# Optimization experiments

Hardware: AMD Instinct MI355X
Metric: run time of the kernel (lower is better)

## Reference

```python
import jax, jax.numpy as jnp
import numpy as np

N_AGENTS = 5
RNN = 128
ATT = 64
N_ACT = 10
IN_DIM = 256
SIZE = 65535  # multiple of N_AGENTS -> padding branch never taken
TAU = 0.01


def _gru_cell(x, h, w_ih, w_hh, b_ih, b_hh):
    # PyTorch GRUCell math
    gi = x @ w_ih.T + b_ih
    gh = h @ w_hh.T + b_hh
    i_r, i_z, i_n = jnp.split(gi, 3, axis=-1)
    h_r, h_z, h_n = jnp.split(gh, 3, axis=-1)
    r = jax.nn.sigmoid(i_r + h_r)
    z = jax.nn.sigmoid(i_z + h_z)
    n = jnp.tanh(i_n + r * h_n)
    return (1.0 - z) * n + z * h


def _gru_seq(xs, w_ih, w_hh, b_ih, b_hh):
    # xs: [T, B, D]; zero initial hidden, returns all step outputs [T, B, RNN]
    h0 = jnp.zeros((xs.shape[1], RNN), xs.dtype)
    def step(h, x):
        h2 = _gru_cell(x, h, w_ih, w_hh, b_ih, b_hh)
        return h2, h2
    _, ys = jax.lax.scan(step, h0, xs)
    return ys


def setup_inputs():
    key = jax.random.key(0)
    ks = jax.random.split(key, 26)
    def u(k, shape, fan):
        return jax.random.uniform(k, shape, jnp.float32, -1.0, 1.0) / np.sqrt(fan)
    return {
        'obs': jax.random.normal(ks[0], (SIZE, IN_DIM), jnp.float32),
        'hidden_state': jax.random.normal(ks[1], (SIZE, RNN), jnp.float32),
        'enc_w': u(ks[2], (RNN, IN_DIM), IN_DIM), 'enc_b': u(ks[3], (RNN,), IN_DIM),
        'gru_w_ih': u(ks[4], (3 * RNN, RNN), RNN), 'gru_w_hh': u(ks[5], (3 * RNN, RNN), RNN),
        'gru_b_ih': u(ks[6], (3 * RNN,), RNN), 'gru_b_hh': u(ks[7], (3 * RNN,), RNN),
        'bi_w_ih_f': u(ks[8], (3 * RNN, 2 * RNN), RNN), 'bi_w_hh_f': u(ks[9], (3 * RNN, RNN), RNN),
        'bi_b_ih_f': u(ks[10], (3 * RNN,), RNN), 'bi_b_hh_f': u(ks[11], (3 * RNN,), RNN),
        'bi_w_ih_r': u(ks[12], (3 * RNN, 2 * RNN), RNN), 'bi_w_hh_r': u(ks[13], (3 * RNN, RNN), RNN),
        'bi_b_ih_r': u(ks[14], (3 * RNN,), RNN), 'bi_b_hh_r': u(ks[15], (3 * RNN,), RNN),
        'hard_w': u(ks[16], (2, 2 * RNN), 2 * RNN), 'hard_b': u(ks[17], (2,), 2 * RNN),
        'q_w': u(ks[18], (ATT, RNN), RNN),
        'k_w': u(ks[19], (ATT, RNN), RNN),
        'v_w': u(ks[20], (ATT, RNN), RNN), 'v_b': u(ks[21], (ATT,), RNN),
        'dec_w': u(ks[22], (N_ACT, RNN + ATT), RNN + ATT), 'dec_b': u(ks[23], (N_ACT,), RNN + ATT),
    }


def reference(obs, hidden_state, enc_w, enc_b, gru_w_ih, gru_w_hh, gru_b_ih, gru_b_hh,
              bi_w_ih_f, bi_w_hh_f, bi_b_ih_f, bi_b_hh_f,
              bi_w_ih_r, bi_w_hh_r, bi_b_ih_r, bi_b_hh_r,
              hard_w, hard_b, q_w, k_w, v_w, v_b, dec_w, dec_b):
    size = obs.shape[0]
    bpa = size // N_AGENTS  # batch per agent; SIZE is a multiple of N_AGENTS

    x = jax.nn.relu(obs @ enc_w.T + enc_b)
    h_out = _gru_cell(x, hidden_state, gru_w_ih, gru_w_hh, gru_b_ih, gru_b_hh)

    # --- hard attention: pairwise agent features -> bi-GRU -> gumbel-softmax gate ---
    # (computed exactly as in the original; note the original soft_attention
    #  ignores hard_weights, so this does not influence the returned output)
    h = h_out.reshape(bpa, N_AGENTS, RNN)
    nbr = np.array([[j for j in range(N_AGENTS) if j != i] for i in range(N_AGENTS)])  # [n, n-1]
    h_i = jnp.broadcast_to(h[:, :, None, :], (bpa, N_AGENTS, N_AGENTS - 1, RNN))
    h_j = h[:, nbr, :]                              # [bpa, n, n-1, RNN]
    pair = jnp.concatenate([h_i, h_j], axis=-1)     # [bpa, n, n-1, 2*RNN]
    seq = pair.transpose(2, 0, 1, 3).reshape(N_AGENTS - 1, bpa * N_AGENTS, 2 * RNN)
    fwd = _gru_seq(seq, bi_w_ih_f, bi_w_hh_f, bi_b_ih_f, bi_b_hh_f)
    bwd = _gru_seq(seq[::-1], bi_w_ih_r, bi_w_hh_r, bi_b_ih_r, bi_b_hh_r)[::-1]
    h_hard = jnp.concatenate([fwd, bwd], axis=-1)   # [n-1, B, 2*RNN]
    h_hard = h_hard.transpose(1, 0, 2).reshape(-1, 2 * RNN)
    logits = h_hard @ hard_w.T + hard_b             # [B*(n-1), 2]
    u01 = jax.random.uniform(jax.random.key(42), logits.shape, jnp.float32, 1e-10, 1.0)
    gumbel = -jnp.log(-jnp.log(u01))
    gs = jax.nn.softmax((logits + gumbel) / TAU, axis=-1)
    hard_weights = gs[:, 1].reshape(bpa, N_AGENTS, 1, N_AGENTS - 1).transpose(1, 0, 2, 3)
    _ = hard_weights  # unused downstream, matching the original module

    # --- soft attention: original loops per sample doing a 1x1 matmul+softmax;
    #     vectorized here. softmax over a single element is identically 1. ---
    q = h_out @ q_w.T
    k = h_out @ k_w.T
    v = jax.nn.relu(h_out @ v_w.T + v_b)
    score = jnp.sum(q * k, axis=-1, keepdims=True) / np.sqrt(ATT)  # [B,1]
    soft_w = jax.nn.softmax(score, axis=-1)                         # all ones
    x_att = v * soft_w

    final_input = jnp.concatenate([h_out, x_att], axis=-1)
    output = final_input @ dec_w.T + dec_b
    return output, h_out
```

## Files before the change

### kernel.cpp

```cpp
#include <hip/hip_runtime.h>
#include <stdint.h>

#define SIZE 65535

typedef __bf16 bf16x8 __attribute__((ext_vector_type(8)));
typedef float floatx4 __attribute__((ext_vector_type(4)));

#define WS_ENCW 0
#define WS_WIH  32768
#define WS_WHH  81920
#define WS_VW   131072
#define WS_DECW 139264
#define WS_TOTC 17792

__device__ __forceinline__ unsigned short f2bf(float f) {
    union { float f; unsigned int u; } v; v.f = f;
    unsigned int u = v.u;
    return (unsigned short)((u + 0x7fffu + ((u >> 16) & 1u)) >> 16);
}
__device__ __forceinline__ float bf2f(unsigned short b) {
    union { unsigned int u; float f; } v; v.u = ((unsigned int)b) << 16;
    return v.f;
}
__device__ __forceinline__ float sigmf(float x) {
    x = fminf(fmaxf(x, -30.f), 30.f);
    return 1.f / (1.f + __expf(-x));
}
__device__ __forceinline__ float tanhfast(float x) {
    x = fminf(fmaxf(x, -15.f), 15.f);
    float e = __expf(2.f * x);
    return (e - 1.f) / (e + 1.f);
}

union BF8 { bf16x8 v; unsigned short s[8]; };

__device__ __forceinline__ bf16x8 cvt8g(const float* p) {
    float4 a = *reinterpret_cast<const float4*>(p);
    float4 b = *reinterpret_cast<const float4*>(p + 4);
    BF8 r;
    r.s[0] = f2bf(a.x); r.s[1] = f2bf(a.y); r.s[2] = f2bf(a.z); r.s[3] = f2bf(a.w);
    r.s[4] = f2bf(b.x); r.s[5] = f2bf(b.y); r.s[6] = f2bf(b.z); r.s[7] = f2bf(b.w);
    return r.v;
}
__device__ __forceinline__ bf16x8 ld8(const unsigned short* p) {
    return *reinterpret_cast<const bf16x8*>(p);
}

__global__ __launch_bounds__(256) void cvt_weights(
    const float* __restrict__ enc_w, const float* __restrict__ w_ih,
    const float* __restrict__ w_hh, const float* __restrict__ v_w,
    const float* __restrict__ dec_w, unsigned short* __restrict__ ws) {
    int c = blockIdx.x * 256 + threadIdx.x;
    if (c >= WS_TOTC) return;
    const int lane = c & 63;
    const int l = lane & 15;
    const int q = lane >> 4;
    const float* src; int row, col, stride; bool zero = false;
    if (c < 4096) {
        int lt = c >> 6; int nt = lt >> 3, kt = lt & 7;
        row = nt * 16 + l; col = kt * 32 + q * 8; src = enc_w; stride = 256;
    } else if (c < 10240) {
        int lt = (c - 4096) >> 6; int nt = lt / 12; int r2 = lt % 12;
        int g = r2 >> 2, kt = r2 & 3;
        row = g * 128 + nt * 16 + l; col = kt * 32 + q * 8; src = w_ih; stride = 128;
    } else if (c < 16384) {
        int lt = (c - 10240) >> 6; int nt = lt / 12; int r2 = lt % 12;
        int g = r2 >> 2, kt = r2 & 3;
        row = g * 128 + nt * 16 + l; col = kt * 32 + q * 8; src = w_hh; stride = 128;
    } else if (c < 17408) {
        int lt = (c - 16384) >> 6; int nt = lt >> 2, kt = lt & 3;
        row = nt * 16 + l; col = kt * 32 + q * 8; src = v_w; stride = 128;
    } else {
        int kt = (c - 17408) >> 6;
        row = l; col = kt * 32 + q * 8; src = dec_w; stride = 192;
        zero = (l >= 10);
    }
    float4 a, b;
    if (zero) { a = make_float4(0.f,0.f,0.f,0.f); b = a; }
    else {
        const float* p = src + (size_t)row * stride + col;
        a = *reinterpret_cast<const float4*>(p);
        b = *reinterpret_cast<const float4*>(p + 4);
    }
    unsigned short* d = ws + (size_t)c * 8;
    d[0]=f2bf(a.x); d[1]=f2bf(a.y); d[2]=f2bf(a.z); d[3]=f2bf(a.w);
    d[4]=f2bf(b.x); d[5]=f2bf(b.y); d[6]=f2bf(b.z); d[7]=f2bf(b.w);
}

__global__ __launch_bounds__(256, 2) void attn_critic_kernel(
    const float* __restrict__ obs,
    const float* __restrict__ hid,
    const float* __restrict__ enc_b,
    const float* __restrict__ b_ih,
    const float* __restrict__ b_hh,
    const float* __restrict__ v_b,
    const float* __restrict__ dec_b,
    const unsigned short* __restrict__ wsw,
    float* __restrict__ out)
{
    __shared__ __align__(16) unsigned short sA[4][32][136];
    __shared__ __align__(16) unsigned short sV[4][32][72];
    __shared__ __align__(16) float sO[4][32][10];

    const int tid  = threadIdx.x;
    const int wave = tid >> 6;
    const int lane = tid & 63;
    const int l15  = lane & 15;
    const int quad = lane >> 4;
    const int wrow0 = (blockIdx.x * 4 + wave) * 32;

    int rA0 = wrow0 + l15;      rA0 = (rA0 < SIZE) ? rA0 : (SIZE - 1);
    int rA1 = wrow0 + 16 + l15; rA1 = (rA1 < SIZE) ? rA1 : (SIZE - 1);

    bf16x8 aob[2][8], hf[2][4];
    {
        const float* o0 = obs + (size_t)rA0 * 256;
        const float* o1 = obs + (size_t)rA1 * 256;
#pragma unroll
        for (int kt = 0; kt < 8; ++kt) {
            aob[0][kt] = cvt8g(o0 + kt * 32 + quad * 8);
            aob[1][kt] = cvt8g(o1 + kt * 32 + quad * 8);
        }
        const float* h0 = hid + (size_t)rA0 * 128;
        const float* h1 = hid + (size_t)rA1 * 128;
#pragma unroll
        for (int kt = 0; kt < 4; ++kt) {
            hf[0][kt] = cvt8g(h0 + kt * 32 + quad * 8);
            hf[1][kt] = cvt8g(h1 + kt * 32 + quad * 8);
        }
    }
    __builtin_amdgcn_sched_barrier(0);

    {
        const unsigned short* encf = wsw + WS_ENCW + lane * 8;
#pragma unroll 2
        for (int nt = 0; nt < 8; ++nt) {
            floatx4 a0 = floatx4{0.f,0.f,0.f,0.f}, a1 = a0;
#pragma unroll
            for (int kt = 0; kt < 8; ++kt) {
                bf16x8 b = ld8(encf + (size_t)(nt * 8 + kt) * 512);
                a0 = __builtin_amdgcn_mfma_f32_16x16x32_bf16(aob[0][kt], b, a0, 0, 0, 0);
                a1 = __builtin_amdgcn_mfma_f32_16x16x32_bf16(aob[1][kt], b, a1, 0, 0, 0);
            }
            float bias = enc_b[nt * 16 + l15];
#pragma unroll
            for (int r = 0; r < 4; ++r) {
                sA[wave][quad * 4 + r][nt * 16 + l15]      = f2bf(fmaxf(a0[r] + bias, 0.f));
                sA[wave][16 + quad * 4 + r][nt * 16 + l15] = f2bf(fmaxf(a1[r] + bias, 0.f));
            }
        }
    }
    bf16x8 xf[2][4];
#pragma unroll
    for (int kt = 0; kt < 4; ++kt) {
        xf[0][kt] = ld8(&sA[wave][l15][kt * 32 + quad * 8]);
        xf[1][kt] = ld8(&sA[wave][16 + l15][kt * 32 + quad * 8]);
    }

    {
        const unsigned short* wihf = wsw + WS_WIH + lane * 8;
        const unsigned short* whhf = wsw + WS_WHH + lane * 8;
#pragma unroll 1
        for (int nt = 0; nt < 8; ++nt) {
            const int nr = nt * 16 + l15;
            floatx4 gi[3][2], gh[3][2];
#pragma unroll
            for (int g = 0; g < 3; ++g) {
                gi[g][0] = floatx4{0.f,0.f,0.f,0.f}; gi[g][1] = gi[g][0];
                gh[g][0] = gi[g][0]; gh[g][1] = gi[g][0];
            }
#pragma unroll
            for (int g = 0; g < 3; ++g)
#pragma unroll
                for (int kt = 0; kt < 4; ++kt) {
                    bf16x8 bi = ld8(wihf + (size_t)((nt * 3 + g) * 4 + kt) * 512);
                    bf16x8 bh = ld8(whhf + (size_t)((nt * 3 + g) * 4 + kt) * 512);
                    gi[g][0] = __builtin_amdgcn_mfma_f32_16x16x32_bf16(xf[0][kt], bi, gi[g][0], 0, 0, 0);
                    gi[g][1] = __builtin_amdgcn_mfma_f32_16x16x32_bf16(xf[1][kt], bi, gi[g][1], 0, 0, 0);
                    gh[g][0] = __builtin_amdgcn_mfma_f32_16x16x32_bf16(hf[0][kt], bh, gh[g][0], 0, 0, 0);
                    gh[g][1] = __builtin_amdgcn_mfma_f32_16x16x32_bf16(hf[1][kt], bh, gh[g][1], 0, 0, 0);
                }
            const float bir_ = b_ih[nr], biz_ = b_ih[nr + 128], bin_ = b_ih[nr + 256];
            const float bhr_ = b_hh[nr], bhz_ = b_hh[nr + 128], bhn_ = b_hh[nr + 256];
#pragma unroll
            for (int m = 0; m < 2; ++m)
#pragma unroll
                for (int r = 0; r < 4; ++r) {
                    const int grow = wrow0 + m * 16 + quad * 4 + r;
                    const int rowc = (grow < SIZE) ? grow : (SIZE - 1);
                    float hprev = hid[(size_t)rowc * 128 + nr];
                    float rg = sigmf(gi[0][m][r] + bir_ + gh[0][m][r] + bhr_);
                    float zg = sigmf(gi[1][m][r] + biz_ + gh[1][m][r] + bhz_);
                    float ng = tanhfast(gi[2][m][r] + bin_ + rg * (gh[2][m][r] + bhn_));
                    float ho = (1.f - zg) * ng + zg * hprev;
                    sA[wave][m * 16 + quad * 4 + r][nr] = f2bf(ho);
                }
        }
    }

    {
        float* out_h = out + (size_t)SIZE * 10;
#pragma unroll 1
        for (int it = 0; it < 16; ++it) {
            int idx = it * 256 + lane * 4;
            int rr = idx >> 7, cc = idx & 127;
            int grow = wrow0 + rr;
            if (grow < SIZE) {
                float2 p0 = make_float2(bf2f(sA[wave][rr][cc]),     bf2f(sA[wave][rr][cc + 1]));
                float2 p1 = make_float2(bf2f(sA[wave][rr][cc + 2]), bf2f(sA[wave][rr][cc + 3]));
                float* dst = out_h + (size_t)grow * 128 + cc;
                *reinterpret_cast<float2*>(dst)     = p0;
                *reinterpret_cast<float2*>(dst + 2) = p1;
            }
        }
    }

    bf16x8 af[2][4];
#pragma unroll
    for (int kt = 0; kt < 4; ++kt) {
        af[0][kt] = ld8(&sA[wave][l15][kt * 32 + quad * 8]);
        af[1][kt] = ld8(&sA[wave][16 + l15][kt * 32 + quad * 8]);
    }
    {
        const unsigned short* vwf = wsw + WS_VW + lane * 8;
#pragma unroll 1
        for (int nt = 0; nt < 4; ++nt) {
            floatx4 a0 = floatx4{0.f,0.f,0.f,0.f}, a1 = a0;
#pragma unroll
            for (int kt = 0; kt < 4; ++kt) {
                bf16x8 b = ld8(vwf + (size_t)(nt * 4 + kt) * 512);
                a0 = __builtin_amdgcn_mfma_f32_16x16x32_bf16(af[0][kt], b, a0, 0, 0, 0);
                a1 = __builtin_amdgcn_mfma_f32_16x16x32_bf16(af[1][kt], b, a1, 0, 0, 0);
            }
            float bias = v_b[nt * 16 + l15];
#pragma unroll
            for (int r = 0; r < 4; ++r) {
                sV[wave][quad * 4 + r][nt * 16 + l15]      = f2bf(fmaxf(a0[r] + bias, 0.f));
                sV[wave][16 + quad * 4 + r][nt * 16 + l15] = f2bf(fmaxf(a1[r] + bias, 0.f));
            }
        }
    }

    {
        const unsigned short* decf = wsw + WS_DECW + lane * 8;
        floatx4 d0 = floatx4{0.f,0.f,0.f,0.f}, d1 = d0;
#pragma unroll
        for (int kt = 0; kt < 6; ++kt) {
            bf16x8 b = ld8(decf + (size_t)kt * 512);
            bf16x8 a0 = (kt < 4) ? af[0][kt] : ld8(&sV[wave][l15][(kt - 4) * 32 + quad * 8]);
            bf16x8 a1 = (kt < 4) ? af[1][kt] : ld8(&sV[wave][16 + l15][(kt - 4) * 32 + quad * 8]);
            d0 = __builtin_amdgcn_mfma_f32_16x16x32_bf16(a0, b, d0, 0, 0, 0);
            d1 = __builtin_amdgcn_mfma_f32_16x16x32_bf16(a1, b, d1, 0, 0, 0);
        }
        if (l15 < 10) {
            float bias = dec_b[l15];
#pragma unroll
            for (int r = 0; r < 4; ++r) {
                sO[wave][quad * 4 + r][l15]      = d0[r] + bias;
                sO[wave][16 + quad * 4 + r][l15] = d1[r] + bias;
            }
        }
#pragma unroll
        for (int j = 0; j < 5; ++j) {
            int idx = j * 64 + lane;
            int row = idx / 10, col = idx % 10;
            int grow = wrow0 + row;
            if (grow < SIZE)
                out[(size_t)grow * 10 + col] = sO[wave][row][col];
        }
    }
}

extern "C" void kernel_launch(void* const* d_in, const int* in_sizes, int n_in,
                              void* d_out, int out_size, void* d_ws, size_t ws_size,
                              hipStream_t stream) {
    const float* obs   = (const float*)d_in[0];
    const float* hid   = (const float*)d_in[1];
    const float* enc_w = (const float*)d_in[2];
    const float* enc_b = (const float*)d_in[3];
    const float* w_ih  = (const float*)d_in[4];
    const float* w_hh  = (const float*)d_in[5];
    const float* b_ih  = (const float*)d_in[6];
    const float* b_hh  = (const float*)d_in[7];
    const float* v_w   = (const float*)d_in[20];
    const float* v_b   = (const float*)d_in[21];
    const float* dec_w = (const float*)d_in[22];
    const float* dec_b = (const float*)d_in[23];
    unsigned short* wsw = (unsigned short*)d_ws;
    float* out = (float*)d_out;

    hipLaunchKernelGGL(cvt_weights, dim3((WS_TOTC + 255) / 256), dim3(256), 0, stream,
                       enc_w, w_ih, w_hh, v_w, dec_w, wsw);
    hipLaunchKernelGGL(attn_critic_kernel, dim3(512), dim3(256), 0, stream,
                       obs, hid, enc_b, b_ih, b_hh, v_b, dec_b, wsw, out);
}
```

Baseline: 224.1 us.

## Split fused critic kernel into three passes with LDS-staged weights

Replaces the single fused kernel with three kernels: an encoder pass that writes bf16 activations to workspace, a GRU pass that splits output columns across four blocks per row tile, and a value/decoder pass that reads back the fp32 hidden output. Each pass stages its weights into LDS via global_load_lds instead of streaming them from global/L2 per wave, and the GRU pass swaps operand order so the output layout allows vectorized float4 stores. This removes the repeated per-wave global weight reads and the serialized long-lived register footprint, at the cost of extra global round trips for the intermediate x and h_out, re-reading hid four times, and added launch overhead.

New measurement: 234.4 us. +4.6%, slower.

```diff
diff --git a/kernel.cpp b/kernel.cpp
--- a/kernel.cpp
+++ b/kernel.cpp
@@ -11,16 +11,13 @@
 #define WS_WHH  81920
 #define WS_VW   131072
 #define WS_DECW 139264
-#define WS_TOTC 17792
+#define WS_TOTC 17920
+#define X_WS    143360
 
 __device__ __forceinline__ unsigned short f2bf(float f) {
     union { float f; unsigned int u; } v; v.f = f;
     unsigned int u = v.u;
     return (unsigned short)((u + 0x7fffu + ((u >> 16) & 1u)) >> 16);
-}
-__device__ __forceinline__ float bf2f(unsigned short b) {
-    union { unsigned int u; float f; } v; v.u = ((unsigned int)b) << 16;
-    return v.f;
 }
 __device__ __forceinline__ float sigmf(float x) {
     x = fminf(fmaxf(x, -30.f), 30.f);
@@ -44,6 +41,11 @@
 }
 __device__ __forceinline__ bf16x8 ld8(const unsigned short* p) {
     return *reinterpret_cast<const bf16x8*>(p);
+}
+__device__ __forceinline__ void glds16(const unsigned short* g, unsigned short* l) {
+    __builtin_amdgcn_global_load_lds(
+        (const __attribute__((address_space(1))) unsigned int*)g,
+        (__attribute__((address_space(3))) unsigned int*)l, 16, 0, 0);
 }
 
 __global__ __launch_bounds__(256) void cvt_weights(
@@ -73,7 +75,7 @@
     } else {
         int kt = (c - 17408) >> 6;
         row = l; col = kt * 32 + q * 8; src = dec_w; stride = 192;
-        zero = (l >= 10);
+        zero = (l >= 10) || (kt >= 6);
     }
     float4 a, b;
     if (zero) { a = make_float4(0.f,0.f,0.f,0.f); b = a; }
@@ -87,18 +89,176 @@
     d[4]=f2bf(b.x); d[5]=f2bf(b.y); d[6]=f2bf(b.z); d[7]=f2bf(b.w);
 }
 
-__global__ __launch_bounds__(256, 2) void attn_critic_kernel(
+__global__ __launch_bounds__(256, 2) void pass1_enc(
     const float* __restrict__ obs,
+    const float* __restrict__ enc_b,
+    const unsigned short* __restrict__ wsw,
+    unsigned short* __restrict__ xws)
+{
+    __shared__ __align__(16) unsigned short wenc[32768];
+
+    const int tid  = threadIdx.x;
+    const int wave = tid >> 6;
+    const int lane = tid & 63;
+    const int l15  = lane & 15;
+    const int quad = lane >> 4;
+    const int wrow0 = blockIdx.x * 128 + wave * 32;
+
+#pragma unroll
+    for (int s = 0; s < 16; ++s) {
+        const int c = s * 256 + tid;
+        glds16(wsw + WS_ENCW + (size_t)c * 8, wenc + (size_t)c * 8);
+    }
+
+    int rA0 = wrow0 + l15;      rA0 = (rA0 < SIZE) ? rA0 : (SIZE - 1);
+    int rA1 = wrow0 + 16 + l15; rA1 = (rA1 < SIZE) ? rA1 : (SIZE - 1);
+
+    bf16x8 bo[2][8];
+    {
+        const float* o0 = obs + (size_t)rA0 * 256;
+        const float* o1 = obs + (size_t)rA1 * 256;
+#pragma unroll
+        for (int kt = 0; kt < 8; ++kt) {
+            bo[0][kt] = cvt8g(o0 + kt * 32 + quad * 8);
+            bo[1][kt] = cvt8g(o1 + kt * 32 + quad * 8);
+        }
+    }
+    __syncthreads();
+
+#pragma unroll 1
+    for (int nt = 0; nt < 8; ++nt) {
+        floatx4 d0 = floatx4{0.f,0.f,0.f,0.f}, d1 = d0;
+#pragma unroll
+        for (int kt = 0; kt < 8; ++kt) {
+            bf16x8 a = ld8(&wenc[(nt * 8 + kt) * 512 + lane * 8]);
+            d0 = __builtin_amdgcn_mfma_f32_16x16x32_bf16(a, bo[0][kt], d0, 0, 0, 0);
+            d1 = __builtin_amdgcn_mfma_f32_16x16x32_bf16(a, bo[1][kt], d1, 0, 0, 0);
+        }
+        const float4 ebv = *reinterpret_cast<const float4*>(enc_b + nt * 16 + quad * 4);
+        const float eb[4] = {ebv.x, ebv.y, ebv.z, ebv.w};
+#pragma unroll
+        for (int m = 0; m < 2; ++m) {
+            const int grow = wrow0 + m * 16 + l15;
+            if (grow < SIZE) {
+                const floatx4& d = m ? d1 : d0;
+                ushort4 pk;
+                pk.x = f2bf(fmaxf(d[0] + eb[0], 0.f));
+                pk.y = f2bf(fmaxf(d[1] + eb[1], 0.f));
+                pk.z = f2bf(fmaxf(d[2] + eb[2], 0.f));
+                pk.w = f2bf(fmaxf(d[3] + eb[3], 0.f));
+                *reinterpret_cast<ushort4*>(xws + (size_t)grow * 128 + nt * 16 + quad * 4) = pk;
+            }
+        }
+    }
+}
+
+__global__ __launch_bounds__(256, 3) void pass2_gru(
     const float* __restrict__ hid,
-    const float* __restrict__ enc_b,
     const float* __restrict__ b_ih,
     const float* __restrict__ b_hh,
+    const unsigned short* __restrict__ wsw,
+    const unsigned short* __restrict__ xws,
+    float* __restrict__ out_h)
+{
+    __shared__ __align__(16) unsigned short wq[24576];
+
+    const int tid  = threadIdx.x;
+    const int wave = tid >> 6;
+    const int lane = tid & 63;
+    const int l15  = lane & 15;
+    const int quad = lane >> 4;
+    const int q    = blockIdx.x & 3;
+    const int tile = blockIdx.x >> 2;
+    const int wrow0 = tile * 128 + wave * 32;
+
+#pragma unroll
+    for (int s = 0; s < 12; ++s) {
+        const int c = s * 256 + tid;
+        const int f = c >> 6, li = c & 63;
+        int ff = (f < 24) ? f : f - 24;
+        const int ntL = ff / 12, rm = ff % 12;
+        const int g = rm >> 2, kt = rm & 3;
+        const int gidx = (((q * 2 + ntL) * 3 + g) * 4 + kt);
+        const unsigned short* src = wsw + ((f < 24) ? WS_WIH : WS_WHH)
+                                        + (size_t)gidx * 512 + li * 8;
+        glds16(src, wq + (size_t)c * 8);
+    }
+
+    int rA0 = wrow0 + l15;      rA0 = (rA0 < SIZE) ? rA0 : (SIZE - 1);
+    int rA1 = wrow0 + 16 + l15; rA1 = (rA1 < SIZE) ? rA1 : (SIZE - 1);
+
+    bf16x8 xb[2][4], hb[2][4];
+#pragma unroll
+    for (int kt = 0; kt < 4; ++kt) {
+        xb[0][kt] = ld8(xws + (size_t)rA0 * 128 + kt * 32 + quad * 8);
+        xb[1][kt] = ld8(xws + (size_t)rA1 * 128 + kt * 32 + quad * 8);
+        hb[0][kt] = cvt8g(hid + (size_t)rA0 * 128 + kt * 32 + quad * 8);
+        hb[1][kt] = cvt8g(hid + (size_t)rA1 * 128 + kt * 32 + quad * 8);
+    }
+    __syncthreads();
+
+#pragma unroll 1
+    for (int ntL = 0; ntL < 2; ++ntL) {
+        const int oc0 = q * 32 + ntL * 16;
+        floatx4 gi[3][2], gh[3][2];
+#pragma unroll
+        for (int g = 0; g < 3; ++g) {
+            gi[g][0] = floatx4{0.f,0.f,0.f,0.f}; gi[g][1] = gi[g][0];
+            gh[g][0] = gi[g][0]; gh[g][1] = gi[g][0];
+        }
+#pragma unroll
+        for (int g = 0; g < 3; ++g)
+#pragma unroll
+            for (int kt = 0; kt < 4; ++kt) {
+                bf16x8 ai = ld8(&wq[((ntL * 3 + g) * 4 + kt) * 512 + lane * 8]);
+                bf16x8 ah = ld8(&wq[12288 + ((ntL * 3 + g) * 4 + kt) * 512 + lane * 8]);
+                gi[g][0] = __builtin_amdgcn_mfma_f32_16x16x32_bf16(ai, xb[0][kt], gi[g][0], 0, 0, 0);
+                gi[g][1] = __builtin_amdgcn_mfma_f32_16x16x32_bf16(ai, xb[1][kt], gi[g][1], 0, 0, 0);
+                gh[g][0] = __builtin_amdgcn_mfma_f32_16x16x32_bf16(ah, hb[0][kt], gh[g][0], 0, 0, 0);
+                gh[g][1] = __builtin_amdgcn_mfma_f32_16x16x32_bf16(ah, hb[1][kt], gh[g][1], 0, 0, 0);
+            }
+        const float4 birv = *reinterpret_cast<const float4*>(b_ih + oc0 + quad * 4);
+        const float4 bizv = *reinterpret_cast<const float4*>(b_ih + 128 + oc0 + quad * 4);
+        const float4 binv = *reinterpret_cast<const float4*>(b_ih + 256 + oc0 + quad * 4);
+        const float4 bhrv = *reinterpret_cast<const float4*>(b_hh + oc0 + quad * 4);
+        const float4 bhzv = *reinterpret_cast<const float4*>(b_hh + 128 + oc0 + quad * 4);
+        const float4 bhnv = *reinterpret_cast<const float4*>(b_hh + 256 + oc0 + quad * 4);
+        const float bir[4] = {birv.x, birv.y, birv.z, birv.w};
+        const float biz[4] = {bizv.x, bizv.y, bizv.z, bizv.w};
+        const float bin[4] = {binv.x, binv.y, binv.z, binv.w};
+        const float bhr[4] = {bhrv.x, bhrv.y, bhrv.z, bhrv.w};
+        const float bhz[4] = {bhzv.x, bhzv.y, bhzv.z, bhzv.w};
+        const float bhn[4] = {bhnv.x, bhnv.y, bhnv.z, bhnv.w};
+#pragma unroll
+        for (int m = 0; m < 2; ++m) {
+            const int grow = wrow0 + m * 16 + l15;
+            const int rowc = (grow < SIZE) ? grow : (SIZE - 1);
+            const float4 hpv = *reinterpret_cast<const float4*>(hid + (size_t)rowc * 128 + oc0 + quad * 4);
+            const float hp[4] = {hpv.x, hpv.y, hpv.z, hpv.w};
+            float ho[4];
+#pragma unroll
+            for (int r = 0; r < 4; ++r) {
+                float rg = sigmf(gi[0][m][r] + bir[r] + gh[0][m][r] + bhr[r]);
+                float zg = sigmf(gi[1][m][r] + biz[r] + gh[1][m][r] + bhz[r]);
+                float ng = tanhfast(gi[2][m][r] + bin[r] + rg * (gh[2][m][r] + bhn[r]));
+                ho[r] = (1.f - zg) * ng + zg * hp[r];
+            }
+            if (grow < SIZE)
+                *reinterpret_cast<float4*>(out_h + (size_t)grow * 128 + oc0 + quad * 4) =
+                    make_float4(ho[0], ho[1], ho[2], ho[3]);
+        }
+    }
+}
+
+__global__ __launch_bounds__(256, 3) void pass3_vdec(
+    const float* __restrict__ hsrc,
     const float* __restrict__ v_b,
     const float* __restrict__ dec_b,
     const unsigned short* __restrict__ wsw,
     float* __restrict__ out)
 {
-    __shared__ __align__(16) unsigned short sA[4][32][136];
+    __shared__ __align__(16) unsigned short wv[8192];
+    __shared__ __align__(16) unsigned short wdec[4096];
     __shared__ __align__(16) unsigned short sV[4][32][72];
     __shared__ __align__(16) float sO[4][32][10];
 
@@ -107,153 +267,59 @@
     const int lane = tid & 63;
     const int l15  = lane & 15;
     const int quad = lane >> 4;
-    const int wrow0 = (blockIdx.x * 4 + wave) * 32;
+    const int wrow0 = blockIdx.x * 128 + wave * 32;
+
+#pragma unroll
+    for (int s = 0; s < 4; ++s) {
+        const int c = s * 256 + tid;
+        glds16(wsw + WS_VW + (size_t)c * 8, wv + (size_t)c * 8);
+    }
+#pragma unroll
+    for (int s = 0; s < 2; ++s) {
+        const int c = s * 256 + tid;
+        glds16(wsw + WS_DECW + (size_t)c * 8, wdec + (size_t)c * 8);
+    }
 
     int rA0 = wrow0 + l15;      rA0 = (rA0 < SIZE) ? rA0 : (SIZE - 1);
     int rA1 = wrow0 + 16 + l15; rA1 = (rA1 < SIZE) ? rA1 : (SIZE - 1);
 
-    bf16x8 aob[2][8], hf[2][4];
+    bf16x8 ha[2][4];
+#pragma unroll
+    for (int kt = 0; kt < 4; ++kt) {
+        ha[0][kt] = cvt8g(hsrc + (size_t)rA0 * 128 + kt * 32 + quad * 8);
+        ha[1][kt] = cvt8g(hsrc + (size_t)rA1 * 128 + kt * 32 + quad * 8);
+    }
+    __syncthreads();
+
+#pragma unroll 1
+    for (int nt = 0; nt < 4; ++nt) {
+        floatx4 a0 = floatx4{0.f,0.f,0.f,0.f}, a1 = a0;
+#pragma unroll
+        for (int kt = 0; kt < 4; ++kt) {
+            bf16x8 b = ld8(&wv[(nt * 4 + kt) * 512 + lane * 8]);
+            a0 = __builtin_amdgcn_mfma_f32_16x16x32_bf16(ha[0][kt], b, a0, 0, 0, 0);
+            a1 = __builtin_amdgcn_mfma_f32_16x16x32_bf16(ha[1][kt], b, a1, 0, 0, 0);
+        }
+        const float bias = v_b[nt * 16 + l15];
+#pragma unroll
+        for (int r = 0; r < 4; ++r) {
+            sV[wave][quad * 4 + r][nt * 16 + l15]      = f2bf(fmaxf(a0[r] + bias, 0.f));
+            sV[wave][16 + quad * 4 + r][nt * 16 + l15] = f2bf(fmaxf(a1[r] + bias, 0.f));
+        }
+    }
+
     {
-        const float* o0 = obs + (size_t)rA0 * 256;
-        const float* o1 = obs + (size_t)rA1 * 256;
-#pragma unroll
-        for (int kt = 0; kt < 8; ++kt) {
-            aob[0][kt] = cvt8g(o0 + kt * 32 + quad * 8);
-            aob[1][kt] = cvt8g(o1 + kt * 32 + quad * 8);
-        }
-        const float* h0 = hid + (size_t)rA0 * 128;
-        const float* h1 = hid + (size_t)rA1 * 128;
-#pragma unroll
-        for (int kt = 0; kt < 4; ++kt) {
-            hf[0][kt] = cvt8g(h0 + kt * 32 + quad * 8);
-            hf[1][kt] = cvt8g(h1 + kt * 32 + quad * 8);
-        }
-    }
-    __builtin_amdgcn_sched_barrier(0);
-
-    {
-        const unsigned short* encf = wsw + WS_ENCW + lane * 8;
-#pragma unroll 2
-        for (int nt = 0; nt < 8; ++nt) {
-            floatx4 a0 = floatx4{0.f,0.f,0.f,0.f}, a1 = a0;
-#pragma unroll
-            for (int kt = 0; kt < 8; ++kt) {
-                bf16x8 b = ld8(encf + (size_t)(nt * 8 + kt) * 512);
-                a0 = __builtin_amdgcn_mfma_f32_16x16x32_bf16(aob[0][kt], b, a0, 0, 0, 0);
-                a1 = __builtin_amdgcn_mfma_f32_16x16x32_bf16(aob[1][kt], b, a1, 0, 0, 0);
-            }
-            float bias = enc_b[nt * 16 + l15];
-#pragma unroll
-            for (int r = 0; r < 4; ++r) {
-                sA[wave][quad * 4 + r][nt * 16 + l15]      = f2bf(fmaxf(a0[r] + bias, 0.f));
-                sA[wave][16 + quad * 4 + r][nt * 16 + l15] = f2bf(fmaxf(a1[r] + bias, 0.f));
-            }
-        }
-    }
-    bf16x8 xf[2][4];
-#pragma unroll
-    for (int kt = 0; kt < 4; ++kt) {
-        xf[0][kt] = ld8(&sA[wave][l15][kt * 32 + quad * 8]);
-        xf[1][kt] = ld8(&sA[wave][16 + l15][kt * 32 + quad * 8]);
-    }
-
-    {
-        const unsigned short* wihf = wsw + WS_WIH + lane * 8;
-        const unsigned short* whhf = wsw + WS_WHH + lane * 8;
-#pragma unroll 1
-        for (int nt = 0; nt < 8; ++nt) {
-            const int nr = nt * 16 + l15;
-            floatx4 gi[3][2], gh[3][2];
-#pragma unroll
-            for (int g = 0; g < 3; ++g) {
-                gi[g][0] = floatx4{0.f,0.f,0.f,0.f}; gi[g][1] = gi[g][0];
-                gh[g][0] = gi[g][0]; gh[g][1] = gi[g][0];
-            }
-#pragma unroll
-            for (int g = 0; g < 3; ++g)
-#pragma unroll
-                for (int kt = 0; kt < 4; ++kt) {
-                    bf16x8 bi = ld8(wihf + (size_t)((nt * 3 + g) * 4 + kt) * 512);
-                    bf16x8 bh = ld8(whhf + (size_t)((nt * 3 + g) * 4 + kt) * 512);
-                    gi[g][0] = __builtin_amdgcn_mfma_f32_16x16x32_bf16(xf[0][kt], bi, gi[g][0], 0, 0, 0);
-                    gi[g][1] = __builtin_amdgcn_mfma_f32_16x16x32_bf16(xf[1][kt], bi, gi[g][1], 0, 0, 0);
-                    gh[g][0] = __builtin_amdgcn_mfma_f32_16x16x32_bf16(hf[0][kt], bh, gh[g][0], 0, 0, 0);
-                    gh[g][1] = __builtin_amdgcn_mfma_f32_16x16x32_bf16(hf[1][kt], bh, gh[g][1], 0, 0, 0);
-                }
-            const float bir_ = b_ih[nr], biz_ = b_ih[nr + 128], bin_ = b_ih[nr + 256];
-            const float bhr_ = b_hh[nr], bhz_ = b_hh[nr + 128], bhn_ = b_hh[nr + 256];
-#pragma unroll
-            for (int m = 0; m < 2; ++m)
-#pragma unroll
-                for (int r = 0; r < 4; ++r) {
-                    const int grow = wrow0 + m * 16 + quad * 4 + r;
-                    const int rowc = (grow < SIZE) ? grow : (SIZE - 1);
-                    float hprev = hid[(size_t)rowc * 128 + nr];
-                    float rg = sigmf(gi[0][m][r] + bir_ + gh[0][m][r] + bhr_);
-                    float zg = sigmf(gi[1][m][r] + biz_ + gh[1][m][r] + bhz_);
-                    float ng = tanhfast(gi[2][m][r] + bin_ + rg * (gh[2][m][r] + bhn_));
-                    float ho = (1.f - zg) * ng + zg * hprev;
-                    sA[wave][m * 16 + quad * 4 + r][nr] = f2bf(ho);
-                }
-        }
-    }
-
-    {
-        float* out_h = out + (size_t)SIZE * 10;
-#pragma unroll 1
-        for (int it = 0; it < 16; ++it) {
-            int idx = it * 256 + lane * 4;
-            int rr = idx >> 7, cc = idx & 127;
-            int grow = wrow0 + rr;
-            if (grow < SIZE) {
-                float2 p0 = make_float2(bf2f(sA[wave][rr][cc]),     bf2f(sA[wave][rr][cc + 1]));
-                float2 p1 = make_float2(bf2f(sA[wave][rr][cc + 2]), bf2f(sA[wave][rr][cc + 3]));
-                float* dst = out_h + (size_t)grow * 128 + cc;
-                *reinterpret_cast<float2*>(dst)     = p0;
-                *reinterpret_cast<float2*>(dst + 2) = p1;
-            }
-        }
-    }
-
-    bf16x8 af[2][4];
-#pragma unroll
-    for (int kt = 0; kt < 4; ++kt) {
-        af[0][kt] = ld8(&sA[wave][l15][kt * 32 + quad * 8]);
-        af[1][kt] = ld8(&sA[wave][16 + l15][kt * 32 + quad * 8]);
-    }
-    {
-        const unsigned short* vwf = wsw + WS_VW + lane * 8;
-#pragma unroll 1
-        for (int nt = 0; nt < 4; ++nt) {
-            floatx4 a0 = floatx4{0.f,0.f,0.f,0.f}, a1 = a0;
-#pragma unroll
-            for (int kt = 0; kt < 4; ++kt) {
-                bf16x8 b = ld8(vwf + (size_t)(nt * 4 + kt) * 512);
-                a0 = __builtin_amdgcn_mfma_f32_16x16x32_bf16(af[0][kt], b, a0, 0, 0, 0);
-                a1 = __builtin_amdgcn_mfma_f32_16x16x32_bf16(af[1][kt], b, a1, 0, 0, 0);
-            }
-            float bias = v_b[nt * 16 + l15];
-#pragma unroll
-            for (int r = 0; r < 4; ++r) {
-                sV[wave][quad * 4 + r][nt * 16 + l15]      = f2bf(fmaxf(a0[r] + bias, 0.f));
-                sV[wave][16 + quad * 4 + r][nt * 16 + l15] = f2bf(fmaxf(a1[r] + bias, 0.f));
-            }
-        }
-    }
-
-    {
-        const unsigned short* decf = wsw + WS_DECW + lane * 8;
         floatx4 d0 = floatx4{0.f,0.f,0.f,0.f}, d1 = d0;
 #pragma unroll
         for (int kt = 0; kt < 6; ++kt) {
-            bf16x8 b = ld8(decf + (size_t)kt * 512);
-            bf16x8 a0 = (kt < 4) ? af[0][kt] : ld8(&sV[wave][l15][(kt - 4) * 32 + quad * 8]);
-            bf16x8 a1 = (kt < 4) ? af[1][kt] : ld8(&sV[wave][16 + l15][(kt - 4) * 32 + quad * 8]);
+            bf16x8 b = ld8(&wdec[kt * 512 + lane * 8]);
+            bf16x8 a0 = (kt < 4) ? ha[0][kt] : ld8(&sV[wave][l15][(kt - 4) * 32 + quad * 8]);
+            bf16x8 a1 = (kt < 4) ? ha[1][kt] : ld8(&sV[wave][16 + l15][(kt - 4) * 32 + quad * 8]);
             d0 = __builtin_amdgcn_mfma_f32_16x16x32_bf16(a0, b, d0, 0, 0, 0);
             d1 = __builtin_amdgcn_mfma_f32_16x16x32_bf16(a1, b, d1, 0, 0, 0);
         }
         if (l15 < 10) {
-            float bias = dec_b[l15];
+            const float bias = dec_b[l15];
 #pragma unroll
             for (int r = 0; r < 4; ++r) {
                 sO[wave][quad * 4 + r][l15]      = d0[r] + bias;
@@ -287,10 +353,16 @@
     const float* dec_w = (const float*)d_in[22];
     const float* dec_b = (const float*)d_in[23];
     unsigned short* wsw = (unsigned short*)d_ws;
-    float* out = (float*)d_out;
+    unsigned short* xws = wsw + X_WS;
+    float* out   = (float*)d_out;
+    float* out_h = out + (size_t)SIZE * 10;
 
     hipLaunchKernelGGL(cvt_weights, dim3((WS_TOTC + 255) / 256), dim3(256), 0, stream,
                        enc_w, w_ih, w_hh, v_w, dec_w, wsw);
-    hipLaunchKernelGGL(attn_critic_kernel, dim3(512), dim3(256), 0, stream,
-                       obs, hid, enc_b, b_ih, b_hh, v_b, dec_b, wsw, out);
-}
+    hipLaunchKernelGGL(pass1_enc, dim3(512), dim3(256), 0, stream,
+                       obs, enc_b, wsw, xws);
+    hipLaunchKernelGGL(pass2_gru, dim3(2048), dim3(256), 0, stream,
+                       hid, b_ih, b_hh, wsw, xws, out_h);
+    hipLaunchKernelGGL(pass3_vdec, dim3(512), dim3(256), 0, stream,
+                       out_h, v_b, dec_b, wsw, out);
+}
```
